# Performance work log

Measured on AMD Instinct MI355X. Metric: run time of the kernel, lower is better.

Reference implementation:

```python
import jax, jax.numpy as jnp
import numpy as np

N_NODES = 100000
N_EDGES = 1600000
IN_DIM = 128
HID = 256
OUT_DIM = 1
NUM_GRAPHS = 2048


def setup_inputs() -> dict:
    key = jax.random.key(0)
    ks = jax.random.split(key, 12)
    x = jax.random.normal(ks[0], (N_NODES, IN_DIM), dtype=jnp.float32)
    edge_index = jax.random.randint(ks[1], (2, N_EDGES), 0, N_NODES, dtype=jnp.int32)
    batch = jnp.sort(jax.random.randint(ks[2], (N_NODES,), 0, NUM_GRAPHS, dtype=jnp.int32))
    def glorot(k, shape):
        lim = float(np.sqrt(6.0 / (shape[0] + shape[1])))
        return jax.random.uniform(k, shape, jnp.float32, -lim, lim)
    W1 = glorot(ks[3], (IN_DIM, HID));  b1 = jnp.zeros((HID,), jnp.float32)
    W2 = glorot(ks[4], (HID, HID));     b2 = jnp.zeros((HID,), jnp.float32)
    Wf1 = glorot(ks[5], (HID, HID // 2)); bf1 = jnp.zeros((HID // 2,), jnp.float32)
    Wf2 = glorot(ks[6], (HID // 2, OUT_DIM)); bf2 = jnp.zeros((OUT_DIM,), jnp.float32)
    return {"x": x, "edge_index": edge_index, "batch": batch,
            "W1": W1, "b1": b1, "W2": W2, "b2": b2,
            "Wf1": Wf1, "bf1": bf1, "Wf2": Wf2, "bf2": bf2}


def _gcn_conv(x, W, b, src, dst, norm, num_nodes):
    # PyG GCNConv: h = X W; out[dst] += norm_e * h[src]; out += b
    h = x @ W                                   # [N, F]
    msg = h[src] * norm[:, None]                # [E', F] gather + scale
    agg = jax.ops.segment_sum(msg, dst, num_segments=num_nodes)
    return agg + b


def reference(x, edge_index, batch, W1, b1, W2, b2, Wf1, bf1, Wf2, bf2):
    n = x.shape[0]
    loop = jnp.arange(n, dtype=edge_index.dtype)
    src = jnp.concatenate([edge_index[0], loop])  # add self-loops (GCN default)
    dst = jnp.concatenate([edge_index[1], loop])
    # symmetric normalization: deg over A+I at dst index
    deg = jax.ops.segment_sum(jnp.ones_like(src, dtype=x.dtype), dst, num_segments=n)
    dinv = jnp.where(deg > 0, jax.lax.rsqrt(deg), 0.0)
    norm = dinv[src] * dinv[dst]                 # [E']

    h = jax.nn.relu(_gcn_conv(x, W1, b1, src, dst, norm, n))
    h = jax.nn.relu(_gcn_conv(h, W2, b2, src, dst, norm, n))

    # global_mean_pool over graphs
    sums = jax.ops.segment_sum(h, batch, num_segments=NUM_GRAPHS)
    cnts = jax.ops.segment_sum(jnp.ones((n,), h.dtype), batch, num_segments=NUM_GRAPHS)
    pooled = sums / jnp.maximum(cnts, 1.0)[:, None]   # [G, HID]

    out = jax.nn.relu(pooled @ Wf1 + bf1) @ Wf2 + bf2  # [G, OUT_DIM]
    return out
```

## Files before the change

### kernel.cpp

```cpp
#include <hip/hip_runtime.h>
#include <hip/hip_bf16.h>

#define N_NODES 100000
#define N_EDGES 1600000
#define IN_DIM 128
#define HID 256
#define NUM_GRAPHS 2048
#define M_PAD 100096
#define SCAN_BLOCKS 98

typedef __bf16 bf16x8 __attribute__((ext_vector_type(8)));
typedef float f32x4 __attribute__((ext_vector_type(4)));

__device__ inline unsigned short f2bf(float x) {
    union { __hip_bfloat16 h; unsigned short u; } v;
    v.h = __float2bfloat16(x);
    return v.u;
}
__device__ inline float bf2f(unsigned short u) {
    return __uint_as_float(((unsigned int)u) << 16);
}

__global__ void count_deg_kernel(const int* __restrict__ ei, int* __restrict__ deg) {
    int e = blockIdx.x * blockDim.x + threadIdx.x;
    if (e < N_EDGES) {
        atomicAdd(&deg[ei[N_EDGES + e]], 1);
    }
}

__global__ __launch_bounds__(1024) void blocksum_kernel(const int* __restrict__ deg,
                                                        int* __restrict__ bsum,
                                                        float* __restrict__ dinv) {
    int i = blockIdx.x * 1024 + threadIdx.x;
    int v = (i < N_NODES) ? deg[i] : 0;
    if (i < N_NODES) dinv[i] = rsqrtf((float)(v + 1));
    __shared__ int s[1024];
    int t = threadIdx.x;
    s[t] = v;
    __syncthreads();
#pragma unroll
    for (int off = 512; off > 0; off >>= 1) {
        if (t < off) s[t] += s[t + off];
        __syncthreads();
    }
    if (t == 0) bsum[blockIdx.x] = s[0];
}

__global__ __launch_bounds__(128) void bscan_kernel(int* __restrict__ bsum) {
    __shared__ int s[128];
    int t = threadIdx.x;
    int v = (t < SCAN_BLOCKS) ? bsum[t] : 0;
    s[t] = v;
    __syncthreads();
#pragma unroll
    for (int off = 1; off < 128; off <<= 1) {
        int x = (t >= off) ? s[t - off] : 0;
        __syncthreads();
        s[t] += x;
        __syncthreads();
    }
    if (t < SCAN_BLOCKS) bsum[t] = (t > 0) ? s[t - 1] : 0;
}

__global__ __launch_bounds__(1024) void scanout_kernel(const int* __restrict__ deg,
                                                       const int* __restrict__ bsum,
                                                       int* __restrict__ rowptr) {
    int i = blockIdx.x * 1024 + threadIdx.x;
    int t = threadIdx.x;
    int v = (i < N_NODES) ? deg[i] : 0;
    __shared__ int s[1024];
    s[t] = v;
    __syncthreads();
#pragma unroll
    for (int off = 1; off < 1024; off <<= 1) {
        int x = (t >= off) ? s[t - off] : 0;
        __syncthreads();
        s[t] += x;
        __syncthreads();
    }
    int base = bsum[blockIdx.x];
    int excl = (t > 0) ? s[t - 1] : 0;
    if (i < N_NODES) rowptr[i] = base + excl;
    if (i == N_NODES - 1) rowptr[N_NODES] = base + s[t];
}

__global__ void fill_kernel(const int* __restrict__ ei, const int* __restrict__ rowptr,
                            int* __restrict__ fill, int* __restrict__ esrc) {
    int e = blockIdx.x * blockDim.x + threadIdx.x;
    if (e < N_EDGES) {
        int dst = ei[N_EDGES + e];
        int pos = rowptr[dst] + atomicAdd(&fill[dst], 1);
        esrc[pos] = ei[e];
    }
}

__global__ void x2bf_kernel(const float* __restrict__ x, unsigned short* __restrict__ xb) {
    size_t i = ((size_t)blockIdx.x * 256 + threadIdx.x) * 4;
    float4 v = *(const float4*)(x + i);
    ushort4 o;
    o.x = f2bf(v.x); o.y = f2bf(v.y); o.z = f2bf(v.z); o.w = f2bf(v.w);
    *(ushort4*)(xb + i) = o;
}

__global__ void wsplit_all_kernel(const float* __restrict__ W1, const float* __restrict__ W2,
                                  unsigned short* __restrict__ W1th, unsigned short* __restrict__ W1tl,
                                  unsigned short* __restrict__ W2th, unsigned short* __restrict__ W2tl) {
    int idx = blockIdx.x * 256 + threadIdx.x;
    if (idx < IN_DIM * 256) {
        int k = idx >> 8, n = idx & 255;
        float w = W1[idx];
        unsigned short h = f2bf(w);
        unsigned short l = f2bf(w - bf2f(h));
        W1th[n * IN_DIM + k] = h;
        W1tl[n * IN_DIM + k] = l;
    } else {
        int i2 = idx - IN_DIM * 256;
        int k = i2 >> 8, n = i2 & 255;
        float w = W2[i2];
        unsigned short h = f2bf(w);
        unsigned short l = f2bf(w - bf2f(h));
        W2th[n * HID + k] = h;
        W2tl[n * HID + k] = l;
    }
}

__global__ __launch_bounds__(256) void agg128_kernel(const unsigned short* __restrict__ X,
                                                     const int* __restrict__ esrc,
                                                     const int* __restrict__ rowptr,
                                                     const float* __restrict__ dinv,
                                                     unsigned short* __restrict__ Ah,
                                                     unsigned short* __restrict__ Al) {
    int node = __builtin_amdgcn_readfirstlane(blockIdx.x * 4 + (threadIdx.x >> 6));
    int lane = threadIdx.x & 63;
    float ddst = dinv[node];
    int s = __builtin_amdgcn_readfirstlane(rowptr[node]);
    int e = __builtin_amdgcn_readfirstlane(rowptr[node + 1]);

    float w0 = ddst * ddst;
    ushort2 h0 = *((const ushort2*)(X + (size_t)node * 128) + lane);
    float2 acc = make_float2(w0 * bf2f(h0.x), w0 * bf2f(h0.y));

    int j = s;
    for (; j + 8 <= e; j += 8) {
        int si[8];
#pragma unroll
        for (int u = 0; u < 8; u++) si[u] = __builtin_amdgcn_readfirstlane(esrc[j + u]);
        ushort2 xv[8];
#pragma unroll
        for (int u = 0; u < 8; u++)
            xv[u] = *((const ushort2*)(X + (size_t)si[u] * 128) + lane);
        float a[8];
#pragma unroll
        for (int u = 0; u < 8; u++) a[u] = dinv[si[u]] * ddst;
#pragma unroll
        for (int u = 0; u < 8; u++) {
            acc.x = fmaf(a[u], bf2f(xv[u].x), acc.x);
            acc.y = fmaf(a[u], bf2f(xv[u].y), acc.y);
        }
    }
    for (; j + 4 <= e; j += 4) {
        int si[4];
#pragma unroll
        for (int u = 0; u < 4; u++) si[u] = __builtin_amdgcn_readfirstlane(esrc[j + u]);
        ushort2 xv[4];
#pragma unroll
        for (int u = 0; u < 4; u++)
            xv[u] = *((const ushort2*)(X + (size_t)si[u] * 128) + lane);
        float a[4];
#pragma unroll
        for (int u = 0; u < 4; u++) a[u] = dinv[si[u]] * ddst;
#pragma unroll
        for (int u = 0; u < 4; u++) {
            acc.x = fmaf(a[u], bf2f(xv[u].x), acc.x);
            acc.y = fmaf(a[u], bf2f(xv[u].y), acc.y);
        }
    }
    for (; j < e; j++) {
        int src = __builtin_amdgcn_readfirstlane(esrc[j]);
        float w = dinv[src] * ddst;
        ushort2 xv = *((const ushort2*)(X + (size_t)src * 128) + lane);
        acc.x = fmaf(w, bf2f(xv.x), acc.x);
        acc.y = fmaf(w, bf2f(xv.y), acc.y);
    }
    size_t o = (size_t)node * 128 + lane * 2;
    ushort2 hi, lo;
    hi.x = f2bf(acc.x); lo.x = f2bf(acc.x - bf2f(hi.x));
    hi.y = f2bf(acc.y); lo.y = f2bf(acc.y - bf2f(hi.y));
    *(ushort2*)(Ah + o) = hi;
    *(ushort2*)(Al + o) = lo;
}

__global__ __launch_bounds__(256) void agg256_kernel(const unsigned short* __restrict__ H,
                                                     const int* __restrict__ esrc,
                                                     const int* __restrict__ rowptr,
                                                     const float* __restrict__ dinv,
                                                     unsigned short* __restrict__ Ah) {
    int node = __builtin_amdgcn_readfirstlane(blockIdx.x * 4 + (threadIdx.x >> 6));
    int lane = threadIdx.x & 63;
    float ddst = dinv[node];
    int s = __builtin_amdgcn_readfirstlane(rowptr[node]);
    int e = __builtin_amdgcn_readfirstlane(rowptr[node + 1]);

    float w0 = ddst * ddst;
    ushort4 h0 = *((const ushort4*)(H + (size_t)node * 256) + lane);
    float4 acc = make_float4(w0 * bf2f(h0.x), w0 * bf2f(h0.y),
                             w0 * bf2f(h0.z), w0 * bf2f(h0.w));

    int j = s;
    for (; j + 8 <= e; j += 8) {
        int si[8];
#pragma unroll
        for (int u = 0; u < 8; u++) si[u] = __builtin_amdgcn_readfirstlane(esrc[j + u]);
        ushort4 xv[8];
#pragma unroll
        for (int u = 0; u < 8; u++)
            xv[u] = *((const ushort4*)(H + (size_t)si[u] * 256) + lane);
        float a[8];
#pragma unroll
        for (int u = 0; u < 8; u++) a[u] = dinv[si[u]] * ddst;
#pragma unroll
        for (int u = 0; u < 8; u++) {
            acc.x = fmaf(a[u], bf2f(xv[u].x), acc.x);
            acc.y = fmaf(a[u], bf2f(xv[u].y), acc.y);
            acc.z = fmaf(a[u], bf2f(xv[u].z), acc.z);
            acc.w = fmaf(a[u], bf2f(xv[u].w), acc.w);
        }
    }
    for (; j + 4 <= e; j += 4) {
        int si[4];
#pragma unroll
        for (int u = 0; u < 4; u++) si[u] = __builtin_amdgcn_readfirstlane(esrc[j + u]);
        ushort4 xv[4];
#pragma unroll
        for (int u = 0; u < 4; u++)
            xv[u] = *((const ushort4*)(H + (size_t)si[u] * 256) + lane);
        float a[4];
#pragma unroll
        for (int u = 0; u < 4; u++) a[u] = dinv[si[u]] * ddst;
#pragma unroll
        for (int u = 0; u < 4; u++) {
            acc.x = fmaf(a[u], bf2f(xv[u].x), acc.x);
            acc.y = fmaf(a[u], bf2f(xv[u].y), acc.y);
            acc.z = fmaf(a[u], bf2f(xv[u].z), acc.z);
            acc.w = fmaf(a[u], bf2f(xv[u].w), acc.w);
        }
    }
    for (; j < e; j++) {
        int src = __builtin_amdgcn_readfirstlane(esrc[j]);
        float w = dinv[src] * ddst;
        ushort4 xv = *((const ushort4*)(H + (size_t)src * 256) + lane);
        acc.x = fmaf(w, bf2f(xv.x), acc.x);
        acc.y = fmaf(w, bf2f(xv.y), acc.y);
        acc.z = fmaf(w, bf2f(xv.z), acc.z);
        acc.w = fmaf(w, bf2f(xv.w), acc.w);
    }
    size_t o = (size_t)node * 256 + lane * 4;
    ushort4 hi;
    hi.x = f2bf(acc.x); hi.y = f2bf(acc.y);
    hi.z = f2bf(acc.z); hi.w = f2bf(acc.w);
    *(ushort4*)(Ah + o) = hi;
}

template <int K, bool ASPLIT>
__launch_bounds__(256, 2)
__global__ void mfma_gemm_bias_relu(const unsigned short* __restrict__ Ah,
                                    const unsigned short* __restrict__ Al,
                                    const unsigned short* __restrict__ Bh,
                                    const unsigned short* __restrict__ Bl,
                                    const float* __restrict__ bias,
                                    unsigned short* __restrict__ Cout) {
    constexpr int NT = ASPLIT ? 4 : 3;
    __shared__ __align__(16) unsigned short lds[NT * 128 * 32];
    unsigned short* Ahs = lds;
    unsigned short* Als = lds + 4096;
    unsigned short* Bhs = lds + (ASPLIT ? 8192 : 4096);
    unsigned short* Bls = lds + (ASPLIT ? 12288 : 8192);

    int tid = threadIdx.x;
    int bm = blockIdx.x * 128;
    int bn = blockIdx.y * 128;
    int wid = tid >> 6, lane = tid & 63;
    int wm = wid & 1, wn = wid >> 1;
    int lrow = lane & 15, quad = lane >> 4;

    f32x4 acc[4][4];
#pragma unroll
    for (int mi = 0; mi < 4; mi++)
#pragma unroll
        for (int ni = 0; ni < 4; ni++) acc[mi][ni] = (f32x4){0.f, 0.f, 0.f, 0.f};

    for (int k0 = 0; k0 < K; k0 += 32) {
#pragma unroll
        for (int i = 0; i < NT * 2; i++) {
            int c = tid + 256 * i;
            int tile = c >> 9;
            int w = c & 511;
            int row = w >> 2;
            int part = w & 3;
            const unsigned short* g;
            if (ASPLIT) {
                if (tile == 0)      g = Ah + (size_t)(bm + row) * K + k0 + part * 8;
                else if (tile == 1) g = Al + (size_t)(bm + row) * K + k0 + part * 8;
                else if (tile == 2) g = Bh + (size_t)(bn + row) * K + k0 + part * 8;
                else                g = Bl + (size_t)(bn + row) * K + k0 + part * 8;
            } else {
                if (tile == 0)      g = Ah + (size_t)(bm + row) * K + k0 + part * 8;
                else if (tile == 1) g = Bh + (size_t)(bn + row) * K + k0 + part * 8;
                else                g = Bl + (size_t)(bn + row) * K + k0 + part * 8;
            }
            ulonglong2 v = *(const ulonglong2*)g;
            *(ulonglong2*)&lds[(tile << 12) + row * 32 + part * 8] = v;
        }
        __syncthreads();

        bf16x8 ah[4], al[4], bh[4], bl[4];
#pragma unroll
        for (int mi = 0; mi < 4; mi++) {
            int r = wm * 64 + mi * 16 + lrow;
            ah[mi] = *(const bf16x8*)&Ahs[r * 32 + quad * 8];
            if (ASPLIT) al[mi] = *(const bf16x8*)&Als[r * 32 + quad * 8];
        }
#pragma unroll
        for (int ni = 0; ni < 4; ni++) {
            int r = wn * 64 + ni * 16 + lrow;
            bh[ni] = *(const bf16x8*)&Bhs[r * 32 + quad * 8];
            bl[ni] = *(const bf16x8*)&Bls[r * 32 + quad * 8];
        }
#pragma unroll
        for (int mi = 0; mi < 4; mi++)
#pragma unroll
            for (int ni = 0; ni < 4; ni++) {
                acc[mi][ni] = __builtin_amdgcn_mfma_f32_16x16x32_bf16(ah[mi], bh[ni], acc[mi][ni], 0, 0, 0);
                acc[mi][ni] = __builtin_amdgcn_mfma_f32_16x16x32_bf16(ah[mi], bl[ni], acc[mi][ni], 0, 0, 0);
                if (ASPLIT)
                    acc[mi][ni] = __builtin_amdgcn_mfma_f32_16x16x32_bf16(al[mi], bh[ni], acc[mi][ni], 0, 0, 0);
            }
        __syncthreads();
    }

    float bv[4];
#pragma unroll
    for (int ni = 0; ni < 4; ni++) bv[ni] = bias[bn + wn * 64 + ni * 16 + lrow];
#pragma unroll
    for (int mi = 0; mi < 4; mi++) {
        int row0 = bm + wm * 64 + mi * 16 + quad * 4;
#pragma unroll
        for (int ni = 0; ni < 4; ni++) {
            int col = bn + wn * 64 + ni * 16 + lrow;
#pragma unroll
            for (int r = 0; r < 4; r++) {
                int row = row0 + r;
                if (row < N_NODES) {
                    float v = fmaxf(acc[mi][ni][r] + bv[ni], 0.f);
                    Cout[(size_t)row * 256 + col] = f2bf(v);
                }
            }
        }
    }
}

__global__ __launch_bounds__(256) void pool_mlp_kernel(const unsigned short* __restrict__ h,
                                                       const int* __restrict__ batch,
                                                       const float* __restrict__ Wf1,
                                                       const float* __restrict__ bf1,
                                                       const float* __restrict__ Wf2,
                                                       const float* __restrict__ bf2,
                                                       float* __restrict__ out) {
    int g = blockIdx.x;
    int t = threadIdx.x;
    __shared__ int bounds[2];
    if (t < 2) {
        int target = g + t;
        int lo = 0, hi = N_NODES;
        while (lo < hi) {
            int mid = (lo + hi) >> 1;
            if (batch[mid] < target) lo = mid + 1;
            else hi = mid;
        }
        bounds[t] = lo;
    }
    __syncthreads();
    int lo = bounds[0], hi = bounds[1];

    float acc = 0.f;
    for (int n = lo; n < hi; n++) acc += bf2f(h[(size_t)n * HID + t]);
    float inv = (hi > lo) ? 1.0f / (float)(hi - lo) : 0.f;
    __shared__ float p[256];
    p[t] = acc * inv;
    __syncthreads();

    float hv = 0.f;
    if (t < 128) {
        float a = bf1[t];
#pragma unroll 8
        for (int k = 0; k < 256; k++) a = fmaf(p[k], Wf1[k * 128 + t], a);
        hv = fmaxf(a, 0.f) * Wf2[t];
    }
#pragma unroll
    for (int off = 32; off > 0; off >>= 1) hv += __shfl_down(hv, off, 64);
    __shared__ float partial[4];
    if ((t & 63) == 0) partial[t >> 6] = hv;
    __syncthreads();
    if (t == 0) out[g] = partial[0] + partial[1] + bf2[0];
}

extern "C" void kernel_launch(void* const* d_in, const int* in_sizes, int n_in,
                              void* d_out, int out_size, void* d_ws, size_t ws_size,
                              hipStream_t stream) {
    const float* x   = (const float*)d_in[0];
    const int*   ei  = (const int*)d_in[1];
    const int*   bat = (const int*)d_in[2];
    const float* W1  = (const float*)d_in[3];
    const float* b1  = (const float*)d_in[4];
    const float* W2  = (const float*)d_in[5];
    const float* b2  = (const float*)d_in[6];
    const float* Wf1 = (const float*)d_in[7];
    const float* bf1 = (const float*)d_in[8];
    const float* Wf2 = (const float*)d_in[9];
    const float* bf2 = (const float*)d_in[10];
    float* out = (float*)d_out;

    char* ws = (char*)d_ws;
    int*   deg    = (int*)(ws);
    float* dinv   = (float*)(ws + 0x0080000);
    int*   rowptr = (int*)(ws + 0x0100000);
    int*   fill   = (int*)(ws + 0x0180000);
    int*   bsum   = (int*)(ws + 0x01F0000);
    int*   esrc   = (int*)(ws + 0x0200000);
    unsigned short* W1th = (unsigned short*)(ws + 0x0820000);
    unsigned short* W1tl = (unsigned short*)(ws + 0x0830000);
    unsigned short* W2th = (unsigned short*)(ws + 0x0840000);
    unsigned short* W2tl = (unsigned short*)(ws + 0x0860000);
    unsigned short* A1h  = (unsigned short*)(ws + 0x0880000);
    unsigned short* A1l  = (unsigned short*)(ws + 0x20F0000);
    unsigned short* A2   = (unsigned short*)(ws + 0x0880000);
    unsigned short* xbf  = (unsigned short*)(ws + 0x6A40000);
    unsigned short* H1bf = (unsigned short*)(ws + 0x6A40000);
    unsigned short* H2bf = (unsigned short*)(ws + 0x6A40000);
    (void)ws_size;

    hipMemsetAsync(deg, 0, (size_t)N_NODES * sizeof(int), stream);
    hipMemsetAsync(fill, 0, (size_t)N_NODES * sizeof(int), stream);

    x2bf_kernel<<<(N_NODES * IN_DIM / 4) / 256, 256, 0, stream>>>(x, xbf);
    wsplit_all_kernel<<<((IN_DIM + HID) * 256) / 256, 256, 0, stream>>>(W1, W2, W1th, W1tl, W2th, W2tl);

    count_deg_kernel<<<(N_EDGES + 255) / 256, 256, 0, stream>>>(ei, deg);
    blocksum_kernel<<<SCAN_BLOCKS, 1024, 0, stream>>>(deg, bsum, dinv);
    bscan_kernel<<<1, 128, 0, stream>>>(bsum);
    scanout_kernel<<<SCAN_BLOCKS, 1024, 0, stream>>>(deg, bsum, rowptr);
    fill_kernel<<<(N_EDGES + 255) / 256, 256, 0, stream>>>(ei, rowptr, fill, esrc);

    agg128_kernel<<<N_NODES / 4, 256, 0, stream>>>(xbf, esrc, rowptr, dinv, A1h, A1l);
    {
        dim3 grid(M_PAD / 128, 2);
        mfma_gemm_bias_relu<IN_DIM, true><<<grid, 256, 0, stream>>>(A1h, A1l, W1th, W1tl, b1, H1bf);
    }

    agg256_kernel<<<N_NODES / 4, 256, 0, stream>>>(H1bf, esrc, rowptr, dinv, A2);
    {
        dim3 grid(M_PAD / 128, 2);
        mfma_gemm_bias_relu<HID, false><<<grid, 256, 0, stream>>>(A2, nullptr, W2th, W2tl, b2, H2bf);
    }

    pool_mlp_kernel<<<NUM_GRAPHS, 256, 0, stream>>>(H2bf, bat, Wf1, bf1, Wf2, bf2, out);
}
```

Before: 598.4 us.

## Widen GEMM tile to full 256 columns and unroll edge gathers by 16

The aggregation kernels now gather 16 neighbor rows per iteration, and the tail is a single masked 16-wide batch that clamps indices and zeroes the weights of out-of-range entries. This replaces the 8/4/1 cascade and raises memory-level parallelism. The GEMM now computes the full 256 output columns per block with a 128x256 tile, so the A tile is loaded once instead of twice across a 2-wide grid. The cost is higher register use (32 accumulators per wave) and more LDS, which may lower occupancy; the launch-bounds hint of 2 blocks is dropped.

```diff
diff --git a/kernel.cpp b/kernel.cpp
--- a/kernel.cpp
+++ b/kernel.cpp
@@ -141,46 +141,43 @@
     float2 acc = make_float2(w0 * bf2f(h0.x), w0 * bf2f(h0.y));
 
     int j = s;
-    for (; j + 8 <= e; j += 8) {
-        int si[8];
-#pragma unroll
-        for (int u = 0; u < 8; u++) si[u] = __builtin_amdgcn_readfirstlane(esrc[j + u]);
-        ushort2 xv[8];
-#pragma unroll
-        for (int u = 0; u < 8; u++)
+    for (; j + 16 <= e; j += 16) {
+        int si[16];
+#pragma unroll
+        for (int u = 0; u < 16; u++) si[u] = __builtin_amdgcn_readfirstlane(esrc[j + u]);
+        ushort2 xv[16];
+#pragma unroll
+        for (int u = 0; u < 16; u++)
             xv[u] = *((const ushort2*)(X + (size_t)si[u] * 128) + lane);
-        float a[8];
-#pragma unroll
-        for (int u = 0; u < 8; u++) a[u] = dinv[si[u]] * ddst;
-#pragma unroll
-        for (int u = 0; u < 8; u++) {
+        float a[16];
+#pragma unroll
+        for (int u = 0; u < 16; u++) a[u] = dinv[si[u]] * ddst;
+#pragma unroll
+        for (int u = 0; u < 16; u++) {
             acc.x = fmaf(a[u], bf2f(xv[u].x), acc.x);
             acc.y = fmaf(a[u], bf2f(xv[u].y), acc.y);
         }
     }
-    for (; j + 4 <= e; j += 4) {
-        int si[4];
-#pragma unroll
-        for (int u = 0; u < 4; u++) si[u] = __builtin_amdgcn_readfirstlane(esrc[j + u]);
-        ushort2 xv[4];
-#pragma unroll
-        for (int u = 0; u < 4; u++)
+    if (j < e) {
+        int si[16];
+#pragma unroll
+        for (int u = 0; u < 16; u++) {
+            int jj = j + u;
+            si[u] = __builtin_amdgcn_readfirstlane(esrc[(jj < e) ? jj : (e - 1)]);
+        }
+        ushort2 xv[16];
+#pragma unroll
+        for (int u = 0; u < 16; u++)
             xv[u] = *((const ushort2*)(X + (size_t)si[u] * 128) + lane);
-        float a[4];
-#pragma unroll
-        for (int u = 0; u < 4; u++) a[u] = dinv[si[u]] * ddst;
-#pragma unroll
-        for (int u = 0; u < 4; u++) {
+        float a[16];
+#pragma unroll
+        for (int u = 0; u < 16; u++)
+            a[u] = (j + u < e) ? dinv[si[u]] * ddst : 0.f;
+#pragma unroll
+        for (int u = 0; u < 16; u++) {
             acc.x = fmaf(a[u], bf2f(xv[u].x), acc.x);
             acc.y = fmaf(a[u], bf2f(xv[u].y), acc.y);
         }
-    }
-    for (; j < e; j++) {
-        int src = __builtin_amdgcn_readfirstlane(esrc[j]);
-        float w = dinv[src] * ddst;
-        ushort2 xv = *((const ushort2*)(X + (size_t)src * 128) + lane);
-        acc.x = fmaf(w, bf2f(xv.x), acc.x);
-        acc.y = fmaf(w, bf2f(xv.y), acc.y);
     }
     size_t o = (size_t)node * 128 + lane * 2;
     ushort2 hi, lo;
@@ -207,52 +204,47 @@
                              w0 * bf2f(h0.z), w0 * bf2f(h0.w));
 
     int j = s;
-    for (; j + 8 <= e; j += 8) {
-        int si[8];
-#pragma unroll
-        for (int u = 0; u < 8; u++) si[u] = __builtin_amdgcn_readfirstlane(esrc[j + u]);
-        ushort4 xv[8];
-#pragma unroll
-        for (int u = 0; u < 8; u++)
+    for (; j + 16 <= e; j += 16) {
+        int si[16];
+#pragma unroll
+        for (int u = 0; u < 16; u++) si[u] = __builtin_amdgcn_readfirstlane(esrc[j + u]);
+        ushort4 xv[16];
+#pragma unroll
+        for (int u = 0; u < 16; u++)
             xv[u] = *((const ushort4*)(H + (size_t)si[u] * 256) + lane);
-        float a[8];
-#pragma unroll
-        for (int u = 0; u < 8; u++) a[u] = dinv[si[u]] * ddst;
-#pragma unroll
-        for (int u = 0; u < 8; u++) {
+        float a[16];
+#pragma unroll
+        for (int u = 0; u < 16; u++) a[u] = dinv[si[u]] * ddst;
+#pragma unroll
+        for (int u = 0; u < 16; u++) {
             acc.x = fmaf(a[u], bf2f(xv[u].x), acc.x);
             acc.y = fmaf(a[u], bf2f(xv[u].y), acc.y);
             acc.z = fmaf(a[u], bf2f(xv[u].z), acc.z);
             acc.w = fmaf(a[u], bf2f(xv[u].w), acc.w);
         }
     }
-    for (; j + 4 <= e; j += 4) {
-        int si[4];
-#pragma unroll
-        for (int u = 0; u < 4; u++) si[u] = __builtin_amdgcn_readfirstlane(esrc[j + u]);
-        ushort4 xv[4];
-#pragma unroll
-        for (int u = 0; u < 4; u++)
+    if (j < e) {
+        int si[16];
+#pragma unroll
+        for (int u = 0; u < 16; u++) {
+            int jj = j + u;
+            si[u] = __builtin_amdgcn_readfirstlane(esrc[(jj < e) ? jj : (e - 1)]);
+        }
+        ushort4 xv[16];
+#pragma unroll
+        for (int u = 0; u < 16; u++)
             xv[u] = *((const ushort4*)(H + (size_t)si[u] * 256) + lane);
-        float a[4];
-#pragma unroll
-        for (int u = 0; u < 4; u++) a[u] = dinv[si[u]] * ddst;
-#pragma unroll
-        for (int u = 0; u < 4; u++) {
+        float a[16];
+#pragma unroll
+        for (int u = 0; u < 16; u++)
+            a[u] = (j + u < e) ? dinv[si[u]] * ddst : 0.f;
+#pragma unroll
+        for (int u = 0; u < 16; u++) {
             acc.x = fmaf(a[u], bf2f(xv[u].x), acc.x);
             acc.y = fmaf(a[u], bf2f(xv[u].y), acc.y);
             acc.z = fmaf(a[u], bf2f(xv[u].z), acc.z);
             acc.w = fmaf(a[u], bf2f(xv[u].w), acc.w);
         }
-    }
-    for (; j < e; j++) {
-        int src = __builtin_amdgcn_readfirstlane(esrc[j]);
-        float w = dinv[src] * ddst;
-        ushort4 xv = *((const ushort4*)(H + (size_t)src * 256) + lane);
-        acc.x = fmaf(w, bf2f(xv.x), acc.x);
-        acc.y = fmaf(w, bf2f(xv.y), acc.y);
-        acc.z = fmaf(w, bf2f(xv.z), acc.z);
-        acc.w = fmaf(w, bf2f(xv.w), acc.w);
     }
     size_t o = (size_t)node * 256 + lane * 4;
     ushort4 hi;
@@ -262,58 +254,62 @@
 }
 
 template <int K, bool ASPLIT>
-__launch_bounds__(256, 2)
+__launch_bounds__(256)
 __global__ void mfma_gemm_bias_relu(const unsigned short* __restrict__ Ah,
                                     const unsigned short* __restrict__ Al,
                                     const unsigned short* __restrict__ Bh,
                                     const unsigned short* __restrict__ Bl,
                                     const float* __restrict__ bias,
                                     unsigned short* __restrict__ Cout) {
-    constexpr int NT = ASPLIT ? 4 : 3;
-    __shared__ __align__(16) unsigned short lds[NT * 128 * 32];
-    unsigned short* Ahs = lds;
-    unsigned short* Als = lds + 4096;
-    unsigned short* Bhs = lds + (ASPLIT ? 8192 : 4096);
-    unsigned short* Bls = lds + (ASPLIT ? 12288 : 8192);
+    __shared__ __align__(16) unsigned short Ahs[128 * 32];
+    __shared__ __align__(16) unsigned short Als[128 * 32];
+    __shared__ __align__(16) unsigned short Bhs[256 * 32];
+    __shared__ __align__(16) unsigned short Bls[256 * 32];
 
     int tid = threadIdx.x;
     int bm = blockIdx.x * 128;
-    int bn = blockIdx.y * 128;
     int wid = tid >> 6, lane = tid & 63;
     int wm = wid & 1, wn = wid >> 1;
     int lrow = lane & 15, quad = lane >> 4;
 
-    f32x4 acc[4][4];
+    f32x4 acc[4][8];
 #pragma unroll
     for (int mi = 0; mi < 4; mi++)
 #pragma unroll
-        for (int ni = 0; ni < 4; ni++) acc[mi][ni] = (f32x4){0.f, 0.f, 0.f, 0.f};
+        for (int ni = 0; ni < 8; ni++) acc[mi][ni] = (f32x4){0.f, 0.f, 0.f, 0.f};
+
+    constexpr int OFF1 = ASPLIT ? 1024 : 512;
+    constexpr int TOT = OFF1 + 2048;
 
     for (int k0 = 0; k0 < K; k0 += 32) {
-#pragma unroll
-        for (int i = 0; i < NT * 2; i++) {
-            int c = tid + 256 * i;
-            int tile = c >> 9;
-            int w = c & 511;
-            int row = w >> 2;
-            int part = w & 3;
+        for (int c = tid; c < TOT; c += 256) {
             const unsigned short* g;
-            if (ASPLIT) {
-                if (tile == 0)      g = Ah + (size_t)(bm + row) * K + k0 + part * 8;
-                else if (tile == 1) g = Al + (size_t)(bm + row) * K + k0 + part * 8;
-                else if (tile == 2) g = Bh + (size_t)(bn + row) * K + k0 + part * 8;
-                else                g = Bl + (size_t)(bn + row) * K + k0 + part * 8;
+            unsigned short* d;
+            if (c < 512) {
+                int row = c >> 2, part = c & 3;
+                g = Ah + (size_t)(bm + row) * K + k0 + part * 8;
+                d = &Ahs[row * 32 + part * 8];
+            } else if (ASPLIT && c < 1024) {
+                int w = c - 512;
+                int row = w >> 2, part = w & 3;
+                g = Al + (size_t)(bm + row) * K + k0 + part * 8;
+                d = &Als[row * 32 + part * 8];
+            } else if (c < OFF1 + 1024) {
+                int w = c - OFF1;
+                int row = w >> 2, part = w & 3;
+                g = Bh + (size_t)row * K + k0 + part * 8;
+                d = &Bhs[row * 32 + part * 8];
             } else {
-                if (tile == 0)      g = Ah + (size_t)(bm + row) * K + k0 + part * 8;
-                else if (tile == 1) g = Bh + (size_t)(bn + row) * K + k0 + part * 8;
-                else                g = Bl + (size_t)(bn + row) * K + k0 + part * 8;
+                int w = c - OFF1 - 1024;
+                int row = w >> 2, part = w & 3;
+                g = Bl + (size_t)row * K + k0 + part * 8;
+                d = &Bls[row * 32 + part * 8];
             }
-            ulonglong2 v = *(const ulonglong2*)g;
-            *(ulonglong2*)&lds[(tile << 12) + row * 32 + part * 8] = v;
-        }
-        __syncthreads();
-
-        bf16x8 ah[4], al[4], bh[4], bl[4];
+            *(ulonglong2*)d = *(const ulonglong2*)g;
+        }
+        __syncthreads();
+
+        bf16x8 ah[4], al[4];
 #pragma unroll
         for (int mi = 0; mi < 4; mi++) {
             int r = wm * 64 + mi * 16 + lrow;
@@ -321,32 +317,30 @@
             if (ASPLIT) al[mi] = *(const bf16x8*)&Als[r * 32 + quad * 8];
         }
 #pragma unroll
-        for (int ni = 0; ni < 4; ni++) {
-            int r = wn * 64 + ni * 16 + lrow;
-            bh[ni] = *(const bf16x8*)&Bhs[r * 32 + quad * 8];
-            bl[ni] = *(const bf16x8*)&Bls[r * 32 + quad * 8];
-        }
-#pragma unroll
-        for (int mi = 0; mi < 4; mi++)
-#pragma unroll
-            for (int ni = 0; ni < 4; ni++) {
-                acc[mi][ni] = __builtin_amdgcn_mfma_f32_16x16x32_bf16(ah[mi], bh[ni], acc[mi][ni], 0, 0, 0);
-                acc[mi][ni] = __builtin_amdgcn_mfma_f32_16x16x32_bf16(ah[mi], bl[ni], acc[mi][ni], 0, 0, 0);
+        for (int ni = 0; ni < 8; ni++) {
+            int rc = wn * 128 + ni * 16 + lrow;
+            bf16x8 bh = *(const bf16x8*)&Bhs[rc * 32 + quad * 8];
+            bf16x8 bl = *(const bf16x8*)&Bls[rc * 32 + quad * 8];
+#pragma unroll
+            for (int mi = 0; mi < 4; mi++) {
+                acc[mi][ni] = __builtin_amdgcn_mfma_f32_16x16x32_bf16(ah[mi], bh, acc[mi][ni], 0, 0, 0);
+                acc[mi][ni] = __builtin_amdgcn_mfma_f32_16x16x32_bf16(ah[mi], bl, acc[mi][ni], 0, 0, 0);
                 if (ASPLIT)
-                    acc[mi][ni] = __builtin_amdgcn_mfma_f32_16x16x32_bf16(al[mi], bh[ni], acc[mi][ni], 0, 0, 0);
+                    acc[mi][ni] = __builtin_amdgcn_mfma_f32_16x16x32_bf16(al[mi], bh, acc[mi][ni], 0, 0, 0);
             }
-        __syncthreads();
-    }
-
-    float bv[4];
-#pragma unroll
-    for (int ni = 0; ni < 4; ni++) bv[ni] = bias[bn + wn * 64 + ni * 16 + lrow];
+        }
+        __syncthreads();
+    }
+
+    float bv[8];
+#pragma unroll
+    for (int ni = 0; ni < 8; ni++) bv[ni] = bias[wn * 128 + ni * 16 + lrow];
 #pragma unroll
     for (int mi = 0; mi < 4; mi++) {
         int row0 = bm + wm * 64 + mi * 16 + quad * 4;
 #pragma unroll
-        for (int ni = 0; ni < 4; ni++) {
-            int col = bn + wn * 64 + ni * 16 + lrow;
+        for (int ni = 0; ni < 8; ni++) {
+            int col = wn * 128 + ni * 16 + lrow;
 #pragma unroll
             for (int r = 0; r < 4; r++) {
                 int row = row0 + r;
@@ -452,16 +446,10 @@
     fill_kernel<<<(N_EDGES + 255) / 256, 256, 0, stream>>>(ei, rowptr, fill, esrc);
 
     agg128_kernel<<<N_NODES / 4, 256, 0, stream>>>(xbf, esrc, rowptr, dinv, A1h, A1l);
-    {
-        dim3 grid(M_PAD / 128, 2);
-        mfma_gemm_bias_relu<IN_DIM, true><<<grid, 256, 0, stream>>>(A1h, A1l, W1th, W1tl, b1, H1bf);
-    }
+    mfma_gemm_bias_relu<IN_DIM, true><<<M_PAD / 128, 256, 0, stream>>>(A1h, A1l, W1th, W1tl, b1, H1bf);
 
     agg256_kernel<<<N_NODES / 4, 256, 0, stream>>>(H1bf, esrc, rowptr, dinv, A2);
-    {
-        dim3 grid(M_PAD / 128, 2);
-        mfma_gemm_bias_relu<HID, false><<<grid, 256, 0, stream>>>(A2, nullptr, W2th, W2tl, b2, H2bf);
-    }
+    mfma_gemm_bias_relu<HID, false><<<M_PAD / 128, 256, 0, stream>>>(A2, nullptr, W2th, W2tl, b2, H2bf);
 
     pool_mlp_kernel<<<NUM_GRAPHS, 256, 0, stream>>>(H2bf, bat, Wf1, bf1, Wf2, bf2, out);
 }
```

New measurement: 734.8 us. 1.23x slower.

## Pre-swizzle weights into MFMA fragment layout and drop LDS staging in GEMM

Applied to the files above, without the earlier changes.

The weight split kernel now writes the hi/lo bf16 weights in a blocked layout that matches the 16x16x32 MFMA operand fragments, so each lane can load its B fragment contiguously. The GEMM no longer stages A and B tiles through shared memory with barriers. Each wave reads its A rows and B fragments directly from global memory into registers, and the launch-bounds occupancy hint is relaxed. This removes LDS traffic and synchronisation, at the cost of redundant global/L2 reads of A across the waves that share rows, and of strided A loads.

```diff
diff --git a/kernel.cpp b/kernel.cpp
--- a/kernel.cpp
+++ b/kernel.cpp
@@ -111,16 +111,18 @@
         float w = W1[idx];
         unsigned short h = f2bf(w);
         unsigned short l = f2bf(w - bf2f(h));
-        W1th[n * IN_DIM + k] = h;
-        W1tl[n * IN_DIM + k] = l;
+        int off = (((n >> 4) * (IN_DIM / 32) + (k >> 5)) * 64 + ((k >> 3) & 3) * 16 + (n & 15)) * 8 + (k & 7);
+        W1th[off] = h;
+        W1tl[off] = l;
     } else {
         int i2 = idx - IN_DIM * 256;
         int k = i2 >> 8, n = i2 & 255;
         float w = W2[i2];
         unsigned short h = f2bf(w);
         unsigned short l = f2bf(w - bf2f(h));
-        W2th[n * HID + k] = h;
-        W2tl[n * HID + k] = l;
+        int off = (((n >> 4) * (HID / 32) + (k >> 5)) * 64 + ((k >> 3) & 3) * 16 + (n & 15)) * 8 + (k & 7);
+        W2th[off] = h;
+        W2tl[off] = l;
     }
 }
 
@@ -262,20 +264,14 @@
 }
 
 template <int K, bool ASPLIT>
-__launch_bounds__(256, 2)
+__launch_bounds__(256)
 __global__ void mfma_gemm_bias_relu(const unsigned short* __restrict__ Ah,
                                     const unsigned short* __restrict__ Al,
                                     const unsigned short* __restrict__ Bh,
                                     const unsigned short* __restrict__ Bl,
                                     const float* __restrict__ bias,
                                     unsigned short* __restrict__ Cout) {
-    constexpr int NT = ASPLIT ? 4 : 3;
-    __shared__ __align__(16) unsigned short lds[NT * 128 * 32];
-    unsigned short* Ahs = lds;
-    unsigned short* Als = lds + 4096;
-    unsigned short* Bhs = lds + (ASPLIT ? 8192 : 4096);
-    unsigned short* Bls = lds + (ASPLIT ? 12288 : 8192);
-
+    constexpr int KC = K / 32;
     int tid = threadIdx.x;
     int bm = blockIdx.x * 128;
     int bn = blockIdx.y * 128;
@@ -289,42 +285,25 @@
 #pragma unroll
         for (int ni = 0; ni < 4; ni++) acc[mi][ni] = (f32x4){0.f, 0.f, 0.f, 0.f};
 
-    for (int k0 = 0; k0 < K; k0 += 32) {
-#pragma unroll
-        for (int i = 0; i < NT * 2; i++) {
-            int c = tid + 256 * i;
-            int tile = c >> 9;
-            int w = c & 511;
-            int row = w >> 2;
-            int part = w & 3;
-            const unsigned short* g;
-            if (ASPLIT) {
-                if (tile == 0)      g = Ah + (size_t)(bm + row) * K + k0 + part * 8;
-                else if (tile == 1) g = Al + (size_t)(bm + row) * K + k0 + part * 8;
-                else if (tile == 2) g = Bh + (size_t)(bn + row) * K + k0 + part * 8;
-                else                g = Bl + (size_t)(bn + row) * K + k0 + part * 8;
-            } else {
-                if (tile == 0)      g = Ah + (size_t)(bm + row) * K + k0 + part * 8;
-                else if (tile == 1) g = Bh + (size_t)(bn + row) * K + k0 + part * 8;
-                else                g = Bl + (size_t)(bn + row) * K + k0 + part * 8;
-            }
-            ulonglong2 v = *(const ulonglong2*)g;
-            *(ulonglong2*)&lds[(tile << 12) + row * 32 + part * 8] = v;
-        }
-        __syncthreads();
-
+    const size_t arow0 = (size_t)(bm + wm * 64 + lrow) * K + quad * 8;
+    const unsigned short* pA = Ah + arow0;
+    const unsigned short* pAl = Al + arow0;
+    const int nb = (bn >> 4) + wn * 4;
+    const unsigned short* pBh = Bh + (size_t)nb * KC * 512 + lane * 8;
+    const unsigned short* pBl = Bl + (size_t)nb * KC * 512 + lane * 8;
+
+#pragma unroll 2
+    for (int kc = 0; kc < KC; kc++) {
         bf16x8 ah[4], al[4], bh[4], bl[4];
 #pragma unroll
         for (int mi = 0; mi < 4; mi++) {
-            int r = wm * 64 + mi * 16 + lrow;
-            ah[mi] = *(const bf16x8*)&Ahs[r * 32 + quad * 8];
-            if (ASPLIT) al[mi] = *(const bf16x8*)&Als[r * 32 + quad * 8];
+            ah[mi] = *(const bf16x8*)(pA + (size_t)mi * 16 * K + kc * 32);
+            if (ASPLIT) al[mi] = *(const bf16x8*)(pAl + (size_t)mi * 16 * K + kc * 32);
         }
 #pragma unroll
         for (int ni = 0; ni < 4; ni++) {
-            int r = wn * 64 + ni * 16 + lrow;
-            bh[ni] = *(const bf16x8*)&Bhs[r * 32 + quad * 8];
-            bl[ni] = *(const bf16x8*)&Bls[r * 32 + quad * 8];
+            bh[ni] = *(const bf16x8*)(pBh + (ni * KC + kc) * 512);
+            bl[ni] = *(const bf16x8*)(pBl + (ni * KC + kc) * 512);
         }
 #pragma unroll
         for (int mi = 0; mi < 4; mi++)
@@ -335,7 +314,6 @@
                 if (ASPLIT)
                     acc[mi][ni] = __builtin_amdgcn_mfma_f32_16x16x32_bf16(al[mi], bh[ni], acc[mi][ni], 0, 0, 0);
             }
-        __syncthreads();
     }
 
     float bv[4];
```

Result: slower. 618.5 us (+3.4%).
